# Performance work log

Hardware: AMD Instinct MI355X
Metric: run time of the kernel (lower is better)

The kernel has to match this reference:

```python
import jax, jax.numpy as jnp
import numpy as np

I3 = jnp.eye(3, dtype=jnp.float32)
G_VEC = jnp.array([0.0, 0.0, -9.80665], dtype=jnp.float32)
# Q diag: [cov_omega x3, cov_acc x3, cov_b_omega x3, cov_b_acc x3, cov_Rot_c_i x3, cov_t_c_i x3]
Q_DIAG = jnp.array([1e-3] * 3 + [1e-2] * 3 + [6e-9] * 3 + [2e-4] * 3 + [1e-9] * 3 + [1e-9] * 3, dtype=jnp.float32)
N_NORM_ROT = 100
N_NORM_ROT_CI = 1000


def skew(v):
    z = jnp.zeros_like(v[0])
    return jnp.stack([jnp.stack([z, -v[2], v[1]]),
                      jnp.stack([v[2], z, -v[0]]),
                      jnp.stack([-v[1], v[0], z])])


def so3exp(phi):
    a2 = jnp.sum(phi * phi)
    small = a2 < 1e-12
    a = jnp.sqrt(jnp.where(small, 1.0, a2))
    axis = phi / a
    c, s = jnp.cos(a), jnp.sin(a)
    big = c * I3 + (1.0 - c) * jnp.outer(axis, axis) + s * skew(axis)
    return jnp.where(small, I3 + skew(phi), big)


def sen3exp(xi):
    # SE_2(3) exponential: xi[:3]=rotation, xi[3:9]=(v, p) parts
    phi = xi[:3]
    a2 = jnp.sum(phi * phi)
    small = a2 < 1e-12
    a = jnp.sqrt(jnp.where(small, 1.0, a2))
    axis = phi / a
    c, s = jnp.cos(a), jnp.sin(a)
    sk = skew(axis)
    R = jnp.where(small, I3 + skew(phi),
                  c * I3 + (1.0 - c) * jnp.outer(axis, axis) + s * sk)
    J = jnp.where(small, I3 + 0.5 * skew(phi),
                  (s / a) * I3 + (1.0 - s / a) * jnp.outer(axis, axis) + ((1.0 - c) / a) * sk)
    x = J @ xi[3:].reshape(2, 3).T  # (3,2): columns are dv, dp
    return R, x


def normalize_rot(R):
    # Polar-factor re-orthonormalization (equivalent to the SVD-based
    # normalize_rot for near-rotation matrices), via Newton-Schulz iteration
    # which is smooth and jit/vjp friendly.
    def body(X, _):
        return 1.5 * X - 0.5 * (X @ X.T @ X), None
    X, _ = jax.lax.scan(body, R, None, length=8)
    return X


def from_rpy(roll, pitch, yaw):
    cr, sr = jnp.cos(roll), jnp.sin(roll)
    cp, sp = jnp.cos(pitch), jnp.sin(pitch)
    cy, sy = jnp.cos(yaw), jnp.sin(yaw)
    one = jnp.ones_like(cr)
    zero = jnp.zeros_like(cr)
    Rx = jnp.stack([jnp.stack([one, zero, zero]), jnp.stack([zero, cr, -sr]), jnp.stack([zero, sr, cr])])
    Ry = jnp.stack([jnp.stack([cp, zero, sp]), jnp.stack([zero, one, zero]), jnp.stack([-sp, zero, cp])])
    Rz = jnp.stack([jnp.stack([cy, -sy, zero]), jnp.stack([sy, cy, zero]), jnp.stack([zero, zero, one])])
    return Rz @ Ry @ Rx


def init_covariance():
    P = jnp.zeros((21, 21), dtype=jnp.float32)
    P = P.at[:2, :2].set(1e-3 * jnp.eye(2))     # cov_Rot0 (no yaw error)
    P = P.at[3:5, 3:5].set(0.1 * jnp.eye(2))    # cov_v0
    P = P.at[9:12, 9:12].set(6e-3 * I3)         # cov_b_omega0
    P = P.at[12:15, 12:15].set(4e-3 * I3)       # cov_b_acc0
    P = P.at[15:18, 15:18].set(1e-6 * I3)       # cov_Rot_c_i0
    P = P.at[18:21, 18:21].set(5e-3 * I3)       # cov_t_c_i0
    return P


def propagate_cov(P, Rot, v, p, dt):
    F = jnp.zeros((21, 21), dtype=P.dtype)
    F = F.at[3:6, :3].set(skew(G_VEC))
    F = F.at[6:9, 3:6].set(I3)
    F = F.at[:3, 9:12].set(-Rot)
    F = F.at[3:6, 9:12].set(-skew(v) @ Rot)
    F = F.at[3:6, 12:15].set(-Rot)
    F = F.at[6:9, 9:12].set(-skew(p) @ Rot)
    G = jnp.zeros((21, 18), dtype=P.dtype)
    G = G.at[:3, :3].set(Rot)
    G = G.at[3:6, 3:6].set(Rot)
    G = G.at[9:12, 6:9].set(I3)
    G = G.at[12:15, 9:12].set(I3)
    G = G.at[15:18, 12:15].set(I3)
    G = G.at[18:21, 15:18].set(I3)
    F = F * dt
    G = G * dt
    F2 = F @ F
    Phi = jnp.eye(21, dtype=P.dtype) + F + 0.5 * F2 + (F2 @ F) / 6.0  # 3rd-order expm
    return Phi @ (P + (G * Q_DIAG[None, :]) @ G.T) @ Phi.T


def _step(carry, xs):
    Rot, v, p, b_om, b_ac, Rci, tci, P = carry
    u_i, dt_i, mcov_i, i = xs
    # ---- propagate ----
    acc = Rot @ (u_i[3:6] - b_ac) + G_VEC
    v_n = v + acc * dt_i
    p_n = p + v * dt_i + 0.5 * acc * dt_i * dt_i
    Rot_n = Rot @ so3exp((u_i[:3] - b_om) * dt_i)
    P_n = propagate_cov(P, Rot, v, p, dt_i)
    # ---- update: zero lateral/vertical body-velocity pseudo-measurement ----
    omega = u_i[:3] - b_om
    Rot_body = Rot_n @ Rci
    v_imu = Rot_n.T @ v_n
    v_body = Rci.T @ v_imu + skew(tci) @ omega
    H = jnp.zeros((2, 21), dtype=P.dtype)
    H = H.at[:, 3:6].set(Rot_body.T[1:])
    H = H.at[:, 15:18].set((Rci.T @ skew(v_imu))[1:])
    H = H.at[:, 9:12].set(skew(tci)[1:])
    H = H.at[:, 18:21].set(-skew(omega)[1:])
    r = -v_body[1:]
    Rm = jnp.diag(mcov_i)
    S = H @ P_n @ H.T + Rm                    # (2,2)
    K = jnp.linalg.solve(S, H @ P_n).T        # K = P H^T S^-1 (P, S symmetric)
    dx = K @ r                                 # (21,)
    dR, dxi = sen3exp(dx[:9])
    Rot_u = dR @ Rot_n
    v_u = dR @ v_n + dxi[:, 0]
    p_u = dR @ p_n + dxi[:, 1]
    b_om_u = b_om + dx[9:12]
    b_ac_u = b_ac + dx[12:15]
    Rci_u = so3exp(dx[15:18]) @ Rci
    tci_u = tci + dx[18:21]
    IKH = jnp.eye(21, dtype=P.dtype) - K @ H
    P_u = IKH @ P_n @ IKH.T + K @ Rm @ K.T    # Joseph form
    P_u = 0.5 * (P_u + P_u.T)
    Rot_u = jnp.where(i % N_NORM_ROT == 0, normalize_rot(Rot_u), Rot_u)
    Rci_u = jnp.where(i % N_NORM_ROT_CI == 0, normalize_rot(Rci_u), Rci_u)
    carry = (Rot_u, v_u, p_u, b_om_u, b_ac_u, Rci_u, tci_u, P_u)
    return carry, (Rot_u, v_u, p_u, b_om_u, b_ac_u, Rci_u, tci_u)


def _forward(t, u, measurements_covs, v_mes, p_mes, ang0, N):
    dt = t[1:N] - t[:N - 1]
    Rot0 = from_rpy(ang0[0], ang0[1], ang0[2])
    z3 = jnp.zeros(3, dtype=u.dtype)
    carry0 = (Rot0, v_mes[0], z3, z3, z3, I3, z3, init_covariance())
    xs = (u[1:N], dt, measurements_covs[1:N], jnp.arange(1, N))
    _, ys = jax.lax.scan(_step, carry0, xs)
    Rot = jnp.concatenate([Rot0[None], ys[0]], axis=0)
    v = jnp.concatenate([v_mes[0][None], ys[1]], axis=0)
    p = jnp.concatenate([z3[None], ys[2]], axis=0)
    b_omega = jnp.concatenate([z3[None], ys[3]], axis=0)
    b_acc = jnp.concatenate([z3[None], ys[4]], axis=0)
    Rot_c_i = jnp.concatenate([I3[None], ys[5]], axis=0)
    t_c_i = jnp.concatenate([z3[None], ys[6]], axis=0)
    return (Rot, v, p, b_omega, b_acc, Rot_c_i, t_c_i)


def setup_inputs() -> dict:
    key = jax.random.key(0)
    N = 20000  # 200 s at 100 Hz IMU
    k0, k1, k2, k3, k4, k5 = jax.random.split(key, 6)
    t = jnp.arange(N, dtype=jnp.float32) * 0.01
    gyro = 0.01 * jax.random.normal(k0, (N, 3), dtype=jnp.float32)
    acc = jnp.array([0.0, 0.0, 9.80665], jnp.float32) + 0.1 * jax.random.normal(k1, (N, 3), dtype=jnp.float32)
    u = jnp.concatenate([gyro, acc], axis=1)
    measurements_covs = 0.1 + jax.random.uniform(k2, (N, 2), dtype=jnp.float32)
    v_mes = jax.random.normal(k3, (N, 3), dtype=jnp.float32)
    p_mes = jax.random.normal(k4, (N, 3), dtype=jnp.float32)
    ang0 = 0.01 * jax.random.normal(k5, (3,), dtype=jnp.float32)
    return dict(t=t, u=u, measurements_covs=measurements_covs, v_mes=v_mes, p_mes=p_mes, ang0=ang0, N=N)


def reference(t, u, measurements_covs, v_mes, p_mes, ang0, N):
    return _forward(t, u, measurements_covs, v_mes, p_mes, ang0, N)
```

## Files before the change

kernel.cpp:

```cpp
#include <hip/hip_runtime.h>

#define GRAV 9.80665f
#define WAVE_SYNC() do { \
    asm volatile("s_waitcnt lgkmcnt(0)" ::: "memory"); \
    __builtin_amdgcn_sched_barrier(0); \
  } while(0)

__device__ __forceinline__ float sel3(int r, float a0, float a1, float a2){
  float x = (r==1)? a1 : a0;
  return (r>=2)? a2 : x;
}

__device__ __forceinline__ void mm33(float* __restrict__ O, const float* A, const float* B){
#pragma unroll
  for(int r=0;r<3;++r){
#pragma unroll
    for(int c=0;c<3;++c){
      O[r*3+c] = A[r*3+0]*B[0*3+c] + A[r*3+1]*B[1*3+c] + A[r*3+2]*B[2*3+c];
    }
  }
}

__device__ __forceinline__ void rot_from_t2(float t_, float p0, float p1, float p2, float* R){
  float c_, k1_, k2_;
  if (t_ < 1e-4f){
    c_  = 1.f - t_*(0.5f - t_*((1.f/24.f) - t_*(1.f/720.f)));
    k2_ = 1.f - t_*((1.f/6.f) - t_*((1.f/120.f) - t_*(1.f/5040.f)));
    k1_ = 0.5f - t_*((1.f/24.f) - t_*(1.f/720.f));
  } else {
    float a = sqrtf(t_);
    c_ = __cosf(a);
    float s = __sinf(a);
    k2_ = s/a;
    k1_ = (1.f - c_)/t_;
  }
  R[0]=c_+k1_*p0*p0;      R[1]=k1_*p0*p1-k2_*p2;  R[2]=k1_*p0*p2+k2_*p1;
  R[3]=k1_*p0*p1+k2_*p2;  R[4]=c_+k1_*p1*p1;      R[5]=k1_*p1*p2-k2_*p0;
  R[6]=k1_*p0*p2-k2_*p1;  R[7]=k1_*p1*p2+k2_*p0;  R[8]=c_+k1_*p2*p2;
}

__device__ __forceinline__ void normalize_rot9(float* X){
#pragma unroll 1
  for(int it=0; it<8; ++it){
    float Y[9], Z[9];
#pragma unroll
    for(int r=0;r<3;++r)
#pragma unroll
      for(int c=0;c<3;++c)
        Y[r*3+c] = X[r*3+0]*X[c*3+0] + X[r*3+1]*X[c*3+1] + X[r*3+2]*X[c*3+2];
#pragma unroll
    for(int r=0;r<3;++r)
#pragma unroll
      for(int c=0;c<3;++c)
        Z[r*3+c] = Y[r*3+0]*X[0*3+c] + Y[r*3+1]*X[1*3+c] + Y[r*3+2]*X[2*3+c];
#pragma unroll
    for(int e=0;e<9;++e) X[e] = 1.5f*X[e] - 0.5f*Z[e];
  }
}

__device__ __forceinline__ float pick_state(int l,
    const float* Rt, const float* vv, const float* pp,
    const float* bw, const float* ba, const float* Rc, const float* tc){
  float s = Rt[0];
  s=(l==1)?Rt[1]:s;  s=(l==2)?Rt[2]:s;  s=(l==3)?Rt[3]:s;  s=(l==4)?Rt[4]:s;
  s=(l==5)?Rt[5]:s;  s=(l==6)?Rt[6]:s;  s=(l==7)?Rt[7]:s;  s=(l==8)?Rt[8]:s;
  s=(l==9)?vv[0]:s;  s=(l==10)?vv[1]:s; s=(l==11)?vv[2]:s;
  s=(l==12)?pp[0]:s; s=(l==13)?pp[1]:s; s=(l==14)?pp[2]:s;
  s=(l==15)?bw[0]:s; s=(l==16)?bw[1]:s; s=(l==17)?bw[2]:s;
  s=(l==18)?ba[0]:s; s=(l==19)?ba[1]:s; s=(l==20)?ba[2]:s;
  s=(l==21)?Rc[0]:s; s=(l==22)?Rc[1]:s; s=(l==23)?Rc[2]:s;
  s=(l==24)?Rc[3]:s; s=(l==25)?Rc[4]:s; s=(l==26)?Rc[5]:s;
  s=(l==27)?Rc[6]:s; s=(l==28)?Rc[7]:s; s=(l==29)?Rc[8]:s;
  s=(l==30)?tc[0]:s; s=(l==31)?tc[1]:s; s=(l==32)?tc[2]:s;
  return s;
}

__global__ __launch_bounds__(64,1)
void iekf_scan_kernel(const float* __restrict__ t,
                      const float* __restrict__ u,
                      const float* __restrict__ mcov,
                      const float* __restrict__ v_mes,
                      const float* __restrict__ ang0,
                      float* __restrict__ out, int N)
{
  const int l = threadIdx.x;
  __shared__ float  Pm[441];
  __shared__ float  Eb[441];
  __shared__ float  PnS[441];
  __shared__ float2 HPs2[21];

  float Rt[9], vv[3], pp[3], bw[3], ba[3], Rc[9], tc[3];
  {
    float rl = ang0[0], pt = ang0[1], yw = ang0[2];
    float cr=cosf(rl), sr=sinf(rl), cp=cosf(pt), sp=sinf(pt), cy=cosf(yw), sy=sinf(yw);
    Rt[0]=cy*cp; Rt[1]=cy*sp*sr - sy*cr; Rt[2]=cy*sp*cr + sy*sr;
    Rt[3]=sy*cp; Rt[4]=sy*sp*sr + cy*cr; Rt[5]=sy*sp*cr - cy*sr;
    Rt[6]=-sp;   Rt[7]=cp*sr;            Rt[8]=cp*cr;
  }
  vv[0]=v_mes[0]; vv[1]=v_mes[1]; vv[2]=v_mes[2];
#pragma unroll
  for(int k=0;k<3;++k){ pp[k]=0.f; bw[k]=0.f; ba[k]=0.f; tc[k]=0.f; }
  Rc[0]=1.f;Rc[1]=0.f;Rc[2]=0.f;Rc[3]=0.f;Rc[4]=1.f;Rc[5]=0.f;Rc[6]=0.f;Rc[7]=0.f;Rc[8]=1.f;

  for (int e=l; e<441; e+=64){
    int r=e/21, c=e-(e/21)*21;
    float vI=0.f;
    if (r==c){
      if (r<2) vI=0.001f;
      else if (r==3||r==4) vI=0.1f;
      else if (r>=9&&r<12) vI=0.006f;
      else if (r>=12&&r<15) vI=0.004f;
      else if (r>=15&&r<18) vI=1e-6f;
      else if (r>=18) vI=0.005f;
    }
    Pm[e]=vI;
  }

  int ostr=0; float* op = out;
  {
    int obase=0, ooff=0;
    if (l<9)       {obase=0;    ostr=9; ooff=l;}
    else if (l<12) {obase=9*N;  ostr=3; ooff=l-9;}
    else if (l<15) {obase=12*N; ostr=3; ooff=l-12;}
    else if (l<18) {obase=15*N; ostr=3; ooff=l-15;}
    else if (l<21) {obase=18*N; ostr=3; ooff=l-18;}
    else if (l<30) {obase=21*N; ostr=9; ooff=l-21;}
    else           {obase=30*N; ostr=3; ooff=l-30;}
    op = out + obase + ooff;
  }

  const int g21 = l/21;
  const int c21 = l - g21*21;
  const int cw  = 9 + 4*g21;
  int l1 = l+21; if (l1>=63) l1-=63;
  int l2 = l+42; if (l2>=63) l2-=63;

  static const int cols[12] = {3,4,5, 9,10,11, 15,16,17, 18,19,20};

  {
    float sv = pick_state(l, Rt, vv, pp, bw, ba, Rc, tc);
    if (l<33) op[0] = sv;
  }
  __syncthreads();

  float tA = t[0], tB = t[1];
  float cu[6];
#pragma unroll
  for(int k=0;k<6;++k) cu[k]=u[6+k];
  float cm0=mcov[2], cm1=mcov[3];

  int nx100=100, nx1000=1000;

#pragma unroll 1
  for (int i=1; i<N; ++i){
    float dt = tB - tA;
    float u0=cu[0], u1=cu[1], u2=cu[2], u3=cu[3], u4=cu[4], u5=cu[5];
    float crm0=cm0, crm1=cm1;
    if (i+1 < N){
      tA = tB; tB = t[i+1];
#pragma unroll
      for(int k=0;k<6;++k) cu[k]=u[(i+1)*6+k];
      cm0 = mcov[(i+1)*2]; cm1 = mcov[(i+1)*2+1];
    }
    float dt2=dt*dt, gdt=GRAV*dt, hdt=0.5f*dt, g6=gdt*dt*(1.0f/6.0f), hdt2=0.5f*dt*dt;

    float w0=u0-bw[0], w1=u1-bw[1], w2=u2-bw[2];
    float aa0=u3-ba[0], aa1=u4-ba[1], aa2=u5-ba[2];
    float acc0 = Rt[0]*aa0+Rt[1]*aa1+Rt[2]*aa2;
    float acc1 = Rt[3]*aa0+Rt[4]*aa1+Rt[5]*aa2;
    float acc2 = Rt[6]*aa0+Rt[7]*aa1+Rt[8]*aa2 - GRAV;
    float vn0=vv[0]+acc0*dt, vn1=vv[1]+acc1*dt, vn2=vv[2]+acc2*dt;
    float pn0=pp[0]+vv[0]*dt+acc0*hdt2;
    float pn1=pp[1]+vv[1]*dt+acc1*hdt2;
    float pn2=pp[2]+vv[2]*dt+acc2*hdt2;
    float ph0=w0*dt, ph1=w1*dt, ph2=w2*dt;
    float dRs[9]; rot_from_t2(ph0*ph0+ph1*ph1+ph2*ph2, ph0,ph1,ph2, dRs);
    float Rn[9]; mm33(Rn, Rt, dRs);
    float Rb[9]; mm33(Rb, Rn, Rc);
    float vi0 = Rn[0]*vn0+Rn[3]*vn1+Rn[6]*vn2;
    float vi1 = Rn[1]*vn0+Rn[4]*vn1+Rn[7]*vn2;
    float vi2 = Rn[2]*vn0+Rn[5]*vn1+Rn[8]*vn2;
    float vb1 = Rc[1]*vi0+Rc[4]*vi1+Rc[7]*vi2 + (tc[2]*w0 - tc[0]*w2);
    float vb2 = Rc[2]*vi0+Rc[5]*vi1+Rc[8]*vi2 + (tc[0]*w1 - tc[1]*w0);
    float rr0 = -vb1, rr1 = -vb2;

    float H0[12], H1[12];
    H0[0]=Rb[1]; H0[1]=Rb[4]; H0[2]=Rb[7];
    H1[0]=Rb[2]; H1[1]=Rb[5]; H1[2]=Rb[8];
    H0[3]=tc[2];  H0[4]=0.f;   H0[5]=-tc[0];
    H1[3]=-tc[1]; H1[4]=tc[0]; H1[5]=0.f;
    H0[6]=Rc[4]*vi2 - Rc[7]*vi1;  H0[7]=Rc[7]*vi0 - Rc[1]*vi2;  H0[8]=Rc[1]*vi1 - Rc[4]*vi0;
    H1[6]=Rc[5]*vi2 - Rc[8]*vi1;  H1[7]=Rc[8]*vi0 - Rc[2]*vi2;  H1[8]=Rc[2]*vi1 - Rc[5]*vi0;
    H0[9]=-w2; H0[10]=0.f; H0[11]=w0;
    H1[9]=w1;  H1[10]=-w0; H1[11]=0.f;

    float Bm[9], Cab[9], D2a[9];
#pragma unroll
    for(int k=0;k<3;++k){
      float b0=-dt*Rt[k], b1=-dt*Rt[3+k], b2=-dt*Rt[6+k];
      float c0=dt*(vv[2]*Rt[3+k]-vv[1]*Rt[6+k]);
      float c1=dt*(vv[0]*Rt[6+k]-vv[2]*Rt[k]);
      float c2=dt*(vv[1]*Rt[k]-vv[0]*Rt[3+k]);
      float d0=dt*(pp[2]*Rt[3+k]-pp[1]*Rt[6+k]);
      float d1=dt*(pp[0]*Rt[6+k]-pp[2]*Rt[k]);
      float d2=dt*(pp[1]*Rt[k]-pp[0]*Rt[3+k]);
      Bm[k]=b0; Bm[3+k]=b1; Bm[6+k]=b2;
      Cab[k]=c0+0.5f*gdt*b1; Cab[3+k]=c1-0.5f*gdt*b0; Cab[6+k]=c2;
      D2a[k]=d0+hdt*c0+g6*b1; D2a[3+k]=d1+hdt*c1-g6*b0; D2a[6+k]=d2+hdt*c2;
    }
    float Bs0=sel3(g21,Bm[0],Bm[3],Bm[6]),  Bs1=sel3(g21,Bm[1],Bm[4],Bm[7]),  Bs2=sel3(g21,Bm[2],Bm[5],Bm[8]);
    float Cs0=sel3(g21,Cab[0],Cab[3],Cab[6]),Cs1=sel3(g21,Cab[1],Cab[4],Cab[7]),Cs2=sel3(g21,Cab[2],Cab[5],Cab[8]);
    float Ds0=sel3(g21,D2a[0],D2a[3],D2a[6]),Ds1=sel3(g21,D2a[1],D2a[4],D2a[7]),Ds2=sel3(g21,D2a[2],D2a[5],D2a[8]);

    float RRT00=Rt[0]*Rt[0]+Rt[1]*Rt[1]+Rt[2]*Rt[2];
    float RRT01=Rt[0]*Rt[3]+Rt[1]*Rt[4]+Rt[2]*Rt[5];
    float RRT02=Rt[0]*Rt[6]+Rt[1]*Rt[7]+Rt[2]*Rt[8];
    float RRT11=Rt[3]*Rt[3]+Rt[4]*Rt[4]+Rt[5]*Rt[5];
    float RRT12=Rt[3]*Rt[6]+Rt[4]*Rt[7]+Rt[5]*Rt[8];
    float RRT22=Rt[6]*Rt[6]+Rt[7]*Rt[7]+Rt[8]*Rt[8];
    float q0d=0.001f*dt2, q1d=0.01f*dt2;
    float q69=6e-9f*dt2, q24=2e-4f*dt2, q19=1e-9f*dt2;

    if (l<63){
      int c = c21;
      bool cl3 = (c<3);
      bool c36 = (c>=3 && c<6);
      float R0c  = sel3(c,   RRT00, RRT01, RRT02);
      float R1c  = sel3(c,   RRT01, RRT11, RRT12);
      float R2c  = sel3(c,   RRT02, RRT12, RRT22);
      float R0c3 = sel3(c-3, RRT00, RRT01, RRT02);
      float R1c3 = sel3(c-3, RRT01, RRT11, RRT12);
      float R2c3 = sel3(c-3, RRT02, RRT12, RRT22);
      float d0  = cl3 ? q0d*R0c : 0.f;
      float d1  = cl3 ? q0d*R1c : 0.f;
      float dg  = cl3 ? q0d*sel3(g21,R0c,R1c,R2c) : 0.f;
      float dg3 = c36 ? q1d*sel3(g21,R0c3,R1c3,R2c3) : 0.f;

      float m0  = Pm[c]            + d0;
      float m1  = Pm[21+c]         + d1;
      float mr  = Pm[g21*21+c]     + dg;
      float m3r = Pm[(3+g21)*21+c] + dg3;
      float m6r = Pm[(6+g21)*21+c];
      float m9  = Pm[9*21+c]  + ((c==9) ? q69 : 0.f);
      float m10 = Pm[10*21+c] + ((c==10)? q69 : 0.f);
      float m11 = Pm[11*21+c] + ((c==11)? q69 : 0.f);
      float m12 = Pm[12*21+c] + ((c==12)? q24 : 0.f);
      float m13 = Pm[13*21+c] + ((c==13)? q24 : 0.f);
      float m14 = Pm[14*21+c] + ((c==14)? q24 : 0.f);

      float Ar = (g21==0)? gdt*m1 : (g21==1)? -gdt*m0 : 0.f;
      float bterm = Bs0*m12+Bs1*m13+Bs2*m14;
      float e0 = mr + Bs0*m9+Bs1*m10+Bs2*m11;
      float e1 = m3r + Ar + Cs0*m9+Cs1*m10+Cs2*m11 + bterm;
      float e2 = m6r + hdt*Ar + dt*m3r + Ds0*m9+Ds1*m10+Ds2*m11 + hdt*bterm;
      Eb[g21*21+c]=e0; Eb[(3+g21)*21+c]=e1; Eb[(6+g21)*21+c]=e2;
#pragma unroll
      for (int jj=0;jj<4;++jj){
        int row = cw+jj;
        float qd = (row<12)? q69 : (row<15)? q24 : q19;
        Eb[row*21+c] = Pm[row*21+c] + ((row==c)? qd : 0.f);
      }
    }
    WAVE_SYNC();

    float pnv[7];
#pragma unroll
    for(int k=0;k<7;++k) pnv[k]=0.f;
    float p0=0.f, p1=0.f;
    if (l<63){
      int r = c21;
      const float* Er = Eb + r*21;
      float e0a=Er[0], e1a=Er[1];
      float eg=Er[g21], e3g=Er[3+g21], e6g=Er[6+g21];
      float e9=Er[9],e10=Er[10],e11=Er[11],e12=Er[12],e13=Er[13],e14=Er[14];
      float Ag = (g21==0)? gdt*e1a : (g21==1)? -gdt*e0a : 0.f;
      float bterm = Bs0*e12+Bs1*e13+Bs2*e14;
      pnv[0] = eg + Bs0*e9+Bs1*e10+Bs2*e11;
      pnv[1] = e3g + Ag + Cs0*e9+Cs1*e10+Cs2*e11 + bterm;
      pnv[2] = e6g + hdt*Ag + dt*e3g + Ds0*e9+Ds1*e10+Ds2*e11 + hdt*bterm;
      pnv[3] = Er[cw]; pnv[4] = Er[cw+1]; pnv[5] = Er[cw+2]; pnv[6] = Er[cw+3];

      PnS[r*21 + g21]     = pnv[0];
      PnS[r*21 + 3+g21]   = pnv[1];
      PnS[r*21 + 6+g21]   = pnv[2];
      PnS[r*21 + cw]      = pnv[3];
      PnS[r*21 + cw+1]    = pnv[4];
      PnS[r*21 + cw+2]    = pnv[5];
      PnS[r*21 + cw+3]    = pnv[6];

      float c1a = sel3(g21, H0[0], H0[1], H0[2]);
      float c3a = sel3(g21, H0[3], 0.f,   H0[8]);
      float c4a = sel3(g21, H0[4], 0.f,   H0[9]);
      float c5a = sel3(g21, H0[5], H0[6], H0[10]);
      float c6a = sel3(g21, 0.f,   H0[7], H0[11]);
      float c1b = sel3(g21, H1[0], H1[1], H1[2]);
      float c3b = sel3(g21, H1[3], 0.f,   H1[8]);
      float c4b = sel3(g21, H1[4], 0.f,   H1[9]);
      float c5b = sel3(g21, H1[5], H1[6], H1[10]);
      float c6b = sel3(g21, 0.f,   H1[7], H1[11]);
      p0 = c1a*pnv[1] + c3a*pnv[3] + c4a*pnv[4] + c5a*pnv[5] + c6a*pnv[6];
      p1 = c1b*pnv[1] + c3b*pnv[3] + c4b*pnv[4] + c5b*pnv[5] + c6b*pnv[6];
    }
    float hpr0 = p0 + __shfl(p0, l1) + __shfl(p0, l2);
    float hpr1 = p1 + __shfl(p1, l1) + __shfl(p1, l2);
    if (l<21) HPs2[c21] = make_float2(hpr0, hpr1);
    WAVE_SYNC();

    float hph00=0.f, hph01=0.f, hph10=0.f, hph11=0.f;
#pragma unroll
    for(int k=0;k<12;++k){
      float2 hp = HPs2[cols[k]];
      hph00 += hp.x*H0[k]; hph01 += hp.x*H1[k];
      hph10 += hp.y*H0[k]; hph11 += hp.y*H1[k];
    }
    float s00 = hph00 + crm0, s01 = hph01, s10 = hph10, s11 = hph11 + crm1;
    float idet = 1.0f/(s00*s11 - s01*s10);
    float i00 =  s11*idet, i01 = -s01*idet, i10 = -s10*idet, i11 = s00*idet;
    float K0 = i00*hpr0 + i01*hpr1;
    float K1 = i10*hpr0 + i11*hpr1;
    float s01q = 0.5f*(s01 + s10);
    float dxval = K0*rr0 + K1*rr1;
    float dxr[21];
    {
      int db = __float_as_int(dxval);
#pragma unroll
      for (int k=0;k<21;++k) dxr[k] = __int_as_float(__builtin_amdgcn_readlane(db, k));
    }

    if (l<63){
      int r = c21;
#pragma unroll
      for (int s=0;s<7;++s){
        int j = (s<3)? (g21 + 3*s) : (cw + (s-3));
        float pnT = PnS[j*21 + r];
        float2 hpj = HPs2[j];
        float kjx = i00*hpj.x + i01*hpj.y;
        float kjy = i10*hpj.x + i11*hpj.y;
        float base  = 0.5f*(pnv[s] + pnT);
        float cross = (K0*hpj.x + K1*hpj.y) + (kjx*hpr0 + kjy*hpr1);
        float quad  = (K0*kjx)*s00 + (K0*kjy + K1*kjx)*s01q + (K1*kjy)*s11;
        Pm[r*21+j] = base - cross + quad;
      }
    }

    float t2x = dxr[0]*dxr[0]+dxr[1]*dxr[1]+dxr[2]*dxr[2];
    float cX,k1X,k2X,j1X;
    if (t2x < 1e-4f){
      cX  = 1.f - t2x*(0.5f - t2x*((1.f/24.f) - t2x*(1.f/720.f)));
      k2X = 1.f - t2x*((1.f/6.f) - t2x*((1.f/120.f) - t2x*(1.f/5040.f)));
      k1X = 0.5f - t2x*((1.f/24.f) - t2x*(1.f/720.f));
      j1X = (1.f/6.f) - t2x*((1.f/120.f) - t2x*(1.f/5040.f));
    } else {
      float a = sqrtf(t2x);
      cX = __cosf(a);
      float s = __sinf(a);
      k2X = s/a; k1X = (1.f-cX)/t2x; j1X = (1.f-k2X)/t2x;
    }
    float dR[9];
    dR[0]=cX+k1X*dxr[0]*dxr[0];      dR[1]=k1X*dxr[0]*dxr[1]-k2X*dxr[2]; dR[2]=k1X*dxr[0]*dxr[2]+k2X*dxr[1];
    dR[3]=k1X*dxr[0]*dxr[1]+k2X*dxr[2]; dR[4]=cX+k1X*dxr[1]*dxr[1];      dR[5]=k1X*dxr[1]*dxr[2]-k2X*dxr[0];
    dR[6]=k1X*dxr[0]*dxr[2]-k2X*dxr[1]; dR[7]=k1X*dxr[1]*dxr[2]+k2X*dxr[0]; dR[8]=cX+k1X*dxr[2]*dxr[2];
    float Jm[9];
    Jm[0]=k2X+j1X*dxr[0]*dxr[0];      Jm[1]=j1X*dxr[0]*dxr[1]-k1X*dxr[2]; Jm[2]=j1X*dxr[0]*dxr[2]+k1X*dxr[1];
    Jm[3]=j1X*dxr[0]*dxr[1]+k1X*dxr[2]; Jm[4]=k2X+j1X*dxr[1]*dxr[1];      Jm[5]=j1X*dxr[1]*dxr[2]-k1X*dxr[0];
    Jm[6]=j1X*dxr[0]*dxr[2]-k1X*dxr[1]; Jm[7]=j1X*dxr[1]*dxr[2]+k1X*dxr[0]; Jm[8]=k2X+j1X*dxr[2]*dxr[2];

    float Ru[9]; mm33(Ru, dR, Rn);
    float vu0 = dR[0]*vn0+dR[1]*vn1+dR[2]*vn2 + Jm[0]*dxr[3]+Jm[1]*dxr[4]+Jm[2]*dxr[5];
    float vu1 = dR[3]*vn0+dR[4]*vn1+dR[5]*vn2 + Jm[3]*dxr[3]+Jm[4]*dxr[4]+Jm[5]*dxr[5];
    float vu2 = dR[6]*vn0+dR[7]*vn1+dR[8]*vn2 + Jm[6]*dxr[3]+Jm[7]*dxr[4]+Jm[8]*dxr[5];
    float pu0 = dR[0]*pn0+dR[1]*pn1+dR[2]*pn2 + Jm[0]*dxr[6]+Jm[1]*dxr[7]+Jm[2]*dxr[8];
    float pu1 = dR[3]*pn0+dR[4]*pn1+dR[5]*pn2 + Jm[3]*dxr[6]+Jm[4]*dxr[7]+Jm[5]*dxr[8];
    float pu2 = dR[6]*pn0+dR[7]*pn1+dR[8]*pn2 + Jm[6]*dxr[6]+Jm[7]*dxr[7]+Jm[8]*dxr[8];
    bw[0]+=dxr[9];  bw[1]+=dxr[10]; bw[2]+=dxr[11];
    ba[0]+=dxr[12]; ba[1]+=dxr[13]; ba[2]+=dxr[14];
    float Ec[9]; rot_from_t2(dxr[15]*dxr[15]+dxr[16]*dxr[16]+dxr[17]*dxr[17], dxr[15],dxr[16],dxr[17], Ec);
    float Rcu[9]; mm33(Rcu, Ec, Rc);
    tc[0]+=dxr[18]; tc[1]+=dxr[19]; tc[2]+=dxr[20];

    if (i==nx100){ normalize_rot9(Ru); nx100+=100; }
    if (i==nx1000){ normalize_rot9(Rcu); nx1000+=1000; }

#pragma unroll
    for(int k=0;k<9;++k){ Rt[k]=Ru[k]; Rc[k]=Rcu[k]; }
    vv[0]=vu0; vv[1]=vu1; vv[2]=vu2;
    pp[0]=pu0; pp[1]=pu1; pp[2]=pu2;

    WAVE_SYNC();

    float sv = pick_state(l, Rt, vv, pp, bw, ba, Rc, tc);
    if (l<33) op[i*ostr] = sv;
  }
}

extern "C" void kernel_launch(void* const* d_in, const int* in_sizes, int n_in,
                              void* d_out, int out_size, void* d_ws, size_t ws_size,
                              hipStream_t stream) {
  (void)n_in; (void)out_size; (void)d_ws; (void)ws_size;
  const float* t     = (const float*)d_in[0];
  const float* u     = (const float*)d_in[1];
  const float* mcov  = (const float*)d_in[2];
  const float* v_mes = (const float*)d_in[3];
  const float* ang0  = (const float*)d_in[5];
  int N = in_sizes[0];
  iekf_scan_kernel<<<dim3(1), dim3(64), 0, stream>>>(t, u, mcov, v_mes, ang0, (float*)d_out, N);
}
```

Measured before the change: 45.60 ms.

## Split filter step across two wavefronts: state propagation vs covariance update

Launches 128 threads as two wavefronts. One wavefront propagates the state, builds H and later applies the correction, while the other computes the covariance propagation and the Kalman update. State, H and the innovation terms now pass through shared memory, with two block-wide barriers per step in place of wave-local syncs. The aim is to run the serial state math alongside the covariance work, at the cost of __syncthreads latency and extra LDS traffic on each of the 20k sequential steps.

```diff
diff --git a/kernel.cpp b/kernel.cpp
--- a/kernel.cpp
+++ b/kernel.cpp
@@ -9,6 +9,19 @@
 __device__ __forceinline__ float sel3(int r, float a0, float a1, float a2){
   float x = (r==1)? a1 : a0;
   return (r>=2)? a2 : x;
+}
+__device__ __forceinline__ float pick12(int k, const float* H){
+  float s=H[0];
+  s=(k==1)?H[1]:s; s=(k==2)?H[2]:s; s=(k==3)?H[3]:s; s=(k==4)?H[4]:s;
+  s=(k==5)?H[5]:s; s=(k==6)?H[6]:s; s=(k==7)?H[7]:s; s=(k==8)?H[8]:s;
+  s=(k==9)?H[9]:s; s=(k==10)?H[10]:s; s=(k==11)?H[11]:s;
+  return s;
+}
+__device__ __forceinline__ float pick9(int k, const float* X){
+  float s=X[0];
+  s=(k==1)?X[1]:s; s=(k==2)?X[2]:s; s=(k==3)?X[3]:s; s=(k==4)?X[4]:s;
+  s=(k==5)?X[5]:s; s=(k==6)?X[6]:s; s=(k==7)?X[7]:s; s=(k==8)?X[8]:s;
+  return s;
 }
 
 __device__ __forceinline__ void mm33(float* __restrict__ O, const float* A, const float* B){
@@ -75,7 +88,7 @@
   return s;
 }
 
-__global__ __launch_bounds__(64,1)
+__global__ __launch_bounds__(128,1)
 void iekf_scan_kernel(const float* __restrict__ t,
                       const float* __restrict__ u,
                       const float* __restrict__ mcov,
@@ -83,26 +96,18 @@
                       const float* __restrict__ ang0,
                       float* __restrict__ out, int N)
 {
-  const int l = threadIdx.x;
+  const int tid = threadIdx.x;
+  const bool isA = (tid < 64);
+  const int l = tid & 63;
+
   __shared__ float  Pm[441];
   __shared__ float  Eb[441];
   __shared__ float  PnS[441];
   __shared__ float2 HPs2[21];
-
-  float Rt[9], vv[3], pp[3], bw[3], ba[3], Rc[9], tc[3];
-  {
-    float rl = ang0[0], pt = ang0[1], yw = ang0[2];
-    float cr=cosf(rl), sr=sinf(rl), cp=cosf(pt), sp=sinf(pt), cy=cosf(yw), sy=sinf(yw);
-    Rt[0]=cy*cp; Rt[1]=cy*sp*sr - sy*cr; Rt[2]=cy*sp*cr + sy*sr;
-    Rt[3]=sy*cp; Rt[4]=sy*sp*sr + cy*cr; Rt[5]=sy*sp*cr - cy*sr;
-    Rt[6]=-sp;   Rt[7]=cp*sr;            Rt[8]=cp*cr;
-  }
-  vv[0]=v_mes[0]; vv[1]=v_mes[1]; vv[2]=v_mes[2];
-#pragma unroll
-  for(int k=0;k<3;++k){ pp[k]=0.f; bw[k]=0.f; ba[k]=0.f; tc[k]=0.f; }
-  Rc[0]=1.f;Rc[1]=0.f;Rc[2]=0.f;Rc[3]=0.f;Rc[4]=1.f;Rc[5]=0.f;Rc[6]=0.f;Rc[7]=0.f;Rc[8]=1.f;
-
-  for (int e=l; e<441; e+=64){
+  __shared__ __align__(16) float stS[36];
+  __shared__ __align__(16) float Hds[24];
+
+  for (int e=tid; e<441; e+=128){
     int r=e/21, c=e-(e/21)*21;
     float vI=0.f;
     if (r==c){
@@ -134,262 +139,376 @@
   const int cw  = 9 + 4*g21;
   int l1 = l+21; if (l1>=63) l1-=63;
   int l2 = l+42; if (l2>=63) l2-=63;
-
   static const int cols[12] = {3,4,5, 9,10,11, 15,16,17, 18,19,20};
 
-  {
-    float sv = pick_state(l, Rt, vv, pp, bw, ba, Rc, tc);
-    if (l<33) op[0] = sv;
+  float tA=0.f, tB=0.f, cu[6]={0,0,0,0,0,0}, cm0=0.f, cm1=0.f;
+
+  if (isA){
+    float Rt0[9], vv0[3], pp0[3], bw0a[3], ba0a[3], Rc0[9], tc0a[3];
+    {
+      float rl = ang0[0], pt = ang0[1], yw = ang0[2];
+      float cr=cosf(rl), sr=sinf(rl), cp=cosf(pt), sp=sinf(pt), cy=cosf(yw), sy=sinf(yw);
+      Rt0[0]=cy*cp; Rt0[1]=cy*sp*sr - sy*cr; Rt0[2]=cy*sp*cr + sy*sr;
+      Rt0[3]=sy*cp; Rt0[4]=sy*sp*sr + cy*cr; Rt0[5]=sy*sp*cr - cy*sr;
+      Rt0[6]=-sp;   Rt0[7]=cp*sr;            Rt0[8]=cp*cr;
+    }
+    vv0[0]=v_mes[0]; vv0[1]=v_mes[1]; vv0[2]=v_mes[2];
+#pragma unroll
+    for(int k=0;k<3;++k){ pp0[k]=0.f; bw0a[k]=0.f; ba0a[k]=0.f; tc0a[k]=0.f; }
+    Rc0[0]=1.f;Rc0[1]=0.f;Rc0[2]=0.f;Rc0[3]=0.f;Rc0[4]=1.f;Rc0[5]=0.f;Rc0[6]=0.f;Rc0[7]=0.f;Rc0[8]=1.f;
+
+    float sv = pick_state(l, Rt0, vv0, pp0, bw0a, ba0a, Rc0, tc0a);
+    if (l<33){ op[0] = sv; stS[l] = sv; }
+
+    tA = t[0]; tB = t[1];
+#pragma unroll
+    for(int k=0;k<6;++k) cu[k]=u[6+k];
+    cm0 = mcov[2]; cm1 = mcov[3];
+    if (l>=33 && l<36) stS[l] = sel3(l-33, tB-tA, cm0, cm1);
   }
   __syncthreads();
-
-  float tA = t[0], tB = t[1];
-  float cu[6];
-#pragma unroll
-  for(int k=0;k<6;++k) cu[k]=u[6+k];
-  float cm0=mcov[2], cm1=mcov[3];
 
   int nx100=100, nx1000=1000;
 
 #pragma unroll 1
   for (int i=1; i<N; ++i){
-    float dt = tB - tA;
-    float u0=cu[0], u1=cu[1], u2=cu[2], u3=cu[3], u4=cu[4], u5=cu[5];
-    float crm0=cm0, crm1=cm1;
-    if (i+1 < N){
-      tA = tB; tB = t[i+1];
-#pragma unroll
-      for(int k=0;k<6;++k) cu[k]=u[(i+1)*6+k];
-      cm0 = mcov[(i+1)*2]; cm1 = mcov[(i+1)*2+1];
+    float Rn[9]; float vn0=0,vn1=0,vn2=0, pn0=0,pn1=0,pn2=0;
+    float H0[12], H1[12];
+    float rr0=0, rr1=0, crm0=0, crm1=0;
+    float bw0=0,bw1=0,bw2=0, ba0=0,ba1=0,ba2=0, tc0=0,tc1=0,tc2=0;
+    float Rc[9];
+    float Bs0=0,Bs1=0,Bs2=0,Cs0=0,Cs1=0,Cs2=0,Ds0=0,Ds1=0,Ds2=0;
+    float dt=0, gdt=0, hdt=0;
+    float pnv[7]; float hpr0=0, hpr1=0;
+#pragma unroll
+    for(int k=0;k<7;++k) pnv[k]=0.f;
+#pragma unroll
+    for(int k=0;k<9;++k){ Rn[k]=0.f; Rc[k]=0.f; }
+#pragma unroll
+    for(int k=0;k<12;++k){ H0[k]=0.f; H1[k]=0.f; }
+
+    if (isA){
+      dt = tB - tA;
+      float u0=cu[0], u1=cu[1], u2=cu[2], u3=cu[3], u4=cu[4], u5=cu[5];
+      crm0=cm0; crm1=cm1;
+      if (i+1 < N){
+        tA = tB; tB = t[i+1];
+#pragma unroll
+        for(int k=0;k<6;++k) cu[k]=u[(i+1)*6+k];
+        cm0 = mcov[(i+1)*2]; cm1 = mcov[(i+1)*2+1];
+      }
+      const float4* st4 = (const float4*)stS;
+      float4 q0=st4[0], q1=st4[1], q2=st4[2], q3=st4[3], q4=st4[4], q5=st4[5], q6=st4[6], q7=st4[7], q8=st4[8];
+      float Rt[9] = {q0.x,q0.y,q0.z,q0.w,q1.x,q1.y,q1.z,q1.w,q2.x};
+      float vv0s=q2.y, vv1s=q2.z, vv2s=q2.w;
+      float pp0s=q3.x, pp1s=q3.y, pp2s=q3.z;
+      bw0=q3.w; bw1=q4.x; bw2=q4.y;
+      ba0=q4.z; ba1=q4.w; ba2=q5.x;
+      Rc[0]=q5.y; Rc[1]=q5.z; Rc[2]=q5.w; Rc[3]=q6.x; Rc[4]=q6.y; Rc[5]=q6.z;
+      Rc[6]=q6.w; Rc[7]=q7.x; Rc[8]=q7.y;
+      tc0=q7.z; tc1=q7.w; tc2=q8.x;
+
+      float hdt2 = 0.5f*dt*dt;
+      float w0=u0-bw0, w1=u1-bw1, w2=u2-bw2;
+      float aa0=u3-ba0, aa1=u4-ba1, aa2=u5-ba2;
+      float acc0 = Rt[0]*aa0+Rt[1]*aa1+Rt[2]*aa2;
+      float acc1 = Rt[3]*aa0+Rt[4]*aa1+Rt[5]*aa2;
+      float acc2 = Rt[6]*aa0+Rt[7]*aa1+Rt[8]*aa2 - GRAV;
+      vn0=vv0s+acc0*dt; vn1=vv1s+acc1*dt; vn2=vv2s+acc2*dt;
+      pn0=pp0s+vv0s*dt+acc0*hdt2;
+      pn1=pp1s+vv1s*dt+acc1*hdt2;
+      pn2=pp2s+vv2s*dt+acc2*hdt2;
+      float ph0=w0*dt, ph1=w1*dt, ph2=w2*dt;
+      float dRs[9]; rot_from_t2(ph0*ph0+ph1*ph1+ph2*ph2, ph0,ph1,ph2, dRs);
+      mm33(Rn, Rt, dRs);
+      float Rb[9]; mm33(Rb, Rn, Rc);
+      float vi0 = Rn[0]*vn0+Rn[3]*vn1+Rn[6]*vn2;
+      float vi1 = Rn[1]*vn0+Rn[4]*vn1+Rn[7]*vn2;
+      float vi2 = Rn[2]*vn0+Rn[5]*vn1+Rn[8]*vn2;
+      float vb1 = Rc[1]*vi0+Rc[4]*vi1+Rc[7]*vi2 + (tc2*w0 - tc0*w2);
+      float vb2 = Rc[2]*vi0+Rc[5]*vi1+Rc[8]*vi2 + (tc0*w1 - tc1*w0);
+      rr0 = -vb1; rr1 = -vb2;
+
+      H0[0]=Rb[1]; H0[1]=Rb[4]; H0[2]=Rb[7];
+      H1[0]=Rb[2]; H1[1]=Rb[5]; H1[2]=Rb[8];
+      H0[3]=tc2;  H0[4]=0.f;  H0[5]=-tc0;
+      H1[3]=-tc1; H1[4]=tc0;  H1[5]=0.f;
+      H0[6]=Rc[4]*vi2 - Rc[7]*vi1;  H0[7]=Rc[7]*vi0 - Rc[1]*vi2;  H0[8]=Rc[1]*vi1 - Rc[4]*vi0;
+      H1[6]=Rc[5]*vi2 - Rc[8]*vi1;  H1[7]=Rc[8]*vi0 - Rc[2]*vi2;  H1[8]=Rc[2]*vi1 - Rc[5]*vi0;
+      H0[9]=-w2; H0[10]=0.f; H0[11]=w0;
+      H1[9]=w1;  H1[10]=-w0; H1[11]=0.f;
+
+      if (l<24){
+        float hv = (l<12)? pick12(l,H0) : pick12(l-12,H1);
+        Hds[l] = hv;
+      }
+    } else {
+      const float4* st4 = (const float4*)stS;
+      float4 q0=st4[0], q1=st4[1], q2=st4[2], q3=st4[3], q8=st4[8];
+      float Rt[9] = {q0.x,q0.y,q0.z,q0.w,q1.x,q1.y,q1.z,q1.w,q2.x};
+      float vv0s=q2.y, vv1s=q2.z, vv2s=q2.w;
+      float pp0s=q3.x, pp1s=q3.y, pp2s=q3.z;
+      dt = q8.y; crm0 = q8.z; crm1 = q8.w;
+      float dt2=dt*dt; gdt=GRAV*dt; hdt=0.5f*dt;
+      float g6=gdt*dt*(1.0f/6.0f);
+
+      float Bm[9], Cab[9], D2a[9];
+#pragma unroll
+      for(int k=0;k<3;++k){
+        float b0=-dt*Rt[k], b1=-dt*Rt[3+k], b2=-dt*Rt[6+k];
+        float c0=dt*(vv2s*Rt[3+k]-vv1s*Rt[6+k]);
+        float c1=dt*(vv0s*Rt[6+k]-vv2s*Rt[k]);
+        float c2=dt*(vv1s*Rt[k]-vv0s*Rt[3+k]);
+        float d0=dt*(pp2s*Rt[3+k]-pp1s*Rt[6+k]);
+        float d1=dt*(pp0s*Rt[6+k]-pp2s*Rt[k]);
+        float d2=dt*(pp1s*Rt[k]-pp0s*Rt[3+k]);
+        Bm[k]=b0; Bm[3+k]=b1; Bm[6+k]=b2;
+        Cab[k]=c0+0.5f*gdt*b1; Cab[3+k]=c1-0.5f*gdt*b0; Cab[6+k]=c2;
+        D2a[k]=d0+hdt*c0+g6*b1; D2a[3+k]=d1+hdt*c1-g6*b0; D2a[6+k]=d2+hdt*c2;
+      }
+      Bs0=sel3(g21,Bm[0],Bm[3],Bm[6]);  Bs1=sel3(g21,Bm[1],Bm[4],Bm[7]);  Bs2=sel3(g21,Bm[2],Bm[5],Bm[8]);
+      Cs0=sel3(g21,Cab[0],Cab[3],Cab[6]);Cs1=sel3(g21,Cab[1],Cab[4],Cab[7]);Cs2=sel3(g21,Cab[2],Cab[5],Cab[8]);
+      Ds0=sel3(g21,D2a[0],D2a[3],D2a[6]);Ds1=sel3(g21,D2a[1],D2a[4],D2a[7]);Ds2=sel3(g21,D2a[2],D2a[5],D2a[8]);
+
+      float RRT00=Rt[0]*Rt[0]+Rt[1]*Rt[1]+Rt[2]*Rt[2];
+      float RRT01=Rt[0]*Rt[3]+Rt[1]*Rt[4]+Rt[2]*Rt[5];
+      float RRT02=Rt[0]*Rt[6]+Rt[1]*Rt[7]+Rt[2]*Rt[8];
+      float RRT11=Rt[3]*Rt[3]+Rt[4]*Rt[4]+Rt[5]*Rt[5];
+      float RRT12=Rt[3]*Rt[6]+Rt[4]*Rt[7]+Rt[5]*Rt[8];
+      float RRT22=Rt[6]*Rt[6]+Rt[7]*Rt[7]+Rt[8]*Rt[8];
+      float q0d=0.001f*dt2, q1d=0.01f*dt2;
+      float q69=6e-9f*dt2, q24=2e-4f*dt2, q19=1e-9f*dt2;
+
+      if (l<63){
+        int c = c21;
+        bool cl3 = (c<3);
+        bool c36 = (c>=3 && c<6);
+        float R0c  = sel3(c,   RRT00, RRT01, RRT02);
+        float R1c  = sel3(c,   RRT01, RRT11, RRT12);
+        float R2c  = sel3(c,   RRT02, RRT12, RRT22);
+        float R0c3 = sel3(c-3, RRT00, RRT01, RRT02);
+        float R1c3 = sel3(c-3, RRT01, RRT11, RRT12);
+        float R2c3 = sel3(c-3, RRT02, RRT12, RRT22);
+        float d0  = cl3 ? q0d*R0c : 0.f;
+        float d1  = cl3 ? q0d*R1c : 0.f;
+        float dg  = cl3 ? q0d*sel3(g21,R0c,R1c,R2c) : 0.f;
+        float dg3 = c36 ? q1d*sel3(g21,R0c3,R1c3,R2c3) : 0.f;
+
+        float m0  = Pm[c]            + d0;
+        float m1  = Pm[21+c]         + d1;
+        float mr  = Pm[g21*21+c]     + dg;
+        float m3r = Pm[(3+g21)*21+c] + dg3;
+        float m6r = Pm[(6+g21)*21+c];
+        float m9  = Pm[9*21+c]  + ((c==9) ? q69 : 0.f);
+        float m10 = Pm[10*21+c] + ((c==10)? q69 : 0.f);
+        float m11 = Pm[11*21+c] + ((c==11)? q69 : 0.f);
+        float m12 = Pm[12*21+c] + ((c==12)? q24 : 0.f);
+        float m13 = Pm[13*21+c] + ((c==13)? q24 : 0.f);
+        float m14 = Pm[14*21+c] + ((c==14)? q24 : 0.f);
+
+        float Ar = (g21==0)? gdt*m1 : (g21==1)? -gdt*m0 : 0.f;
+        float bterm = Bs0*m12+Bs1*m13+Bs2*m14;
+        float e0 = mr + Bs0*m9+Bs1*m10+Bs2*m11;
+        float e1 = m3r + Ar + Cs0*m9+Cs1*m10+Cs2*m11 + bterm;
+        float e2 = m6r + hdt*Ar + dt*m3r + Ds0*m9+Ds1*m10+Ds2*m11 + hdt*bterm;
+        Eb[g21*21+c]=e0; Eb[(3+g21)*21+c]=e1; Eb[(6+g21)*21+c]=e2;
+#pragma unroll
+        for (int jj=0;jj<4;++jj){
+          int row = cw+jj;
+          float qd = (row<12)? q69 : (row<15)? q24 : q19;
+          Eb[row*21+c] = Pm[row*21+c] + ((row==c)? qd : 0.f);
+        }
+      }
     }
-    float dt2=dt*dt, gdt=GRAV*dt, hdt=0.5f*dt, g6=gdt*dt*(1.0f/6.0f), hdt2=0.5f*dt*dt;
-
-    float w0=u0-bw[0], w1=u1-bw[1], w2=u2-bw[2];
-    float aa0=u3-ba[0], aa1=u4-ba[1], aa2=u5-ba[2];
-    float acc0 = Rt[0]*aa0+Rt[1]*aa1+Rt[2]*aa2;
-    float acc1 = Rt[3]*aa0+Rt[4]*aa1+Rt[5]*aa2;
-    float acc2 = Rt[6]*aa0+Rt[7]*aa1+Rt[8]*aa2 - GRAV;
-    float vn0=vv[0]+acc0*dt, vn1=vv[1]+acc1*dt, vn2=vv[2]+acc2*dt;
-    float pn0=pp[0]+vv[0]*dt+acc0*hdt2;
-    float pn1=pp[1]+vv[1]*dt+acc1*hdt2;
-    float pn2=pp[2]+vv[2]*dt+acc2*hdt2;
-    float ph0=w0*dt, ph1=w1*dt, ph2=w2*dt;
-    float dRs[9]; rot_from_t2(ph0*ph0+ph1*ph1+ph2*ph2, ph0,ph1,ph2, dRs);
-    float Rn[9]; mm33(Rn, Rt, dRs);
-    float Rb[9]; mm33(Rb, Rn, Rc);
-    float vi0 = Rn[0]*vn0+Rn[3]*vn1+Rn[6]*vn2;
-    float vi1 = Rn[1]*vn0+Rn[4]*vn1+Rn[7]*vn2;
-    float vi2 = Rn[2]*vn0+Rn[5]*vn1+Rn[8]*vn2;
-    float vb1 = Rc[1]*vi0+Rc[4]*vi1+Rc[7]*vi2 + (tc[2]*w0 - tc[0]*w2);
-    float vb2 = Rc[2]*vi0+Rc[5]*vi1+Rc[8]*vi2 + (tc[0]*w1 - tc[1]*w0);
-    float rr0 = -vb1, rr1 = -vb2;
-
-    float H0[12], H1[12];
-    H0[0]=Rb[1]; H0[1]=Rb[4]; H0[2]=Rb[7];
-    H1[0]=Rb[2]; H1[1]=Rb[5]; H1[2]=Rb[8];
-    H0[3]=tc[2];  H0[4]=0.f;   H0[5]=-tc[0];
-    H1[3]=-tc[1]; H1[4]=tc[0]; H1[5]=0.f;
-    H0[6]=Rc[4]*vi2 - Rc[7]*vi1;  H0[7]=Rc[7]*vi0 - Rc[1]*vi2;  H0[8]=Rc[1]*vi1 - Rc[4]*vi0;
-    H1[6]=Rc[5]*vi2 - Rc[8]*vi1;  H1[7]=Rc[8]*vi0 - Rc[2]*vi2;  H1[8]=Rc[2]*vi1 - Rc[5]*vi0;
-    H0[9]=-w2; H0[10]=0.f; H0[11]=w0;
-    H1[9]=w1;  H1[10]=-w0; H1[11]=0.f;
-
-    float Bm[9], Cab[9], D2a[9];
-#pragma unroll
-    for(int k=0;k<3;++k){
-      float b0=-dt*Rt[k], b1=-dt*Rt[3+k], b2=-dt*Rt[6+k];
-      float c0=dt*(vv[2]*Rt[3+k]-vv[1]*Rt[6+k]);
-      float c1=dt*(vv[0]*Rt[6+k]-vv[2]*Rt[k]);
-      float c2=dt*(vv[1]*Rt[k]-vv[0]*Rt[3+k]);
-      float d0=dt*(pp[2]*Rt[3+k]-pp[1]*Rt[6+k]);
-      float d1=dt*(pp[0]*Rt[6+k]-pp[2]*Rt[k]);
-      float d2=dt*(pp[1]*Rt[k]-pp[0]*Rt[3+k]);
-      Bm[k]=b0; Bm[3+k]=b1; Bm[6+k]=b2;
-      Cab[k]=c0+0.5f*gdt*b1; Cab[3+k]=c1-0.5f*gdt*b0; Cab[6+k]=c2;
-      D2a[k]=d0+hdt*c0+g6*b1; D2a[3+k]=d1+hdt*c1-g6*b0; D2a[6+k]=d2+hdt*c2;
+    __syncthreads();
+
+    if (!isA){
+      const float4* h4p = (const float4*)Hds;
+      float4 h0v=h4p[0], h1v=h4p[1], h2v=h4p[2], h3v=h4p[3], h4v=h4p[4], h5v=h4p[5];
+      H0[0]=h0v.x; H0[1]=h0v.y; H0[2]=h0v.z; H0[3]=h0v.w;
+      H0[4]=h1v.x; H0[5]=h1v.y; H0[6]=h1v.z; H0[7]=h1v.w;
+      H0[8]=h2v.x; H0[9]=h2v.y; H0[10]=h2v.z; H0[11]=h2v.w;
+      H1[0]=h3v.x; H1[1]=h3v.y; H1[2]=h3v.z; H1[3]=h3v.w;
+      H1[4]=h4v.x; H1[5]=h4v.y; H1[6]=h4v.z; H1[7]=h4v.w;
+      H1[8]=h5v.x; H1[9]=h5v.y; H1[10]=h5v.z; H1[11]=h5v.w;
+
+      float p0=0.f, p1=0.f;
+      if (l<63){
+        int r = c21;
+        const float* Er = Eb + r*21;
+        float e0a=Er[0], e1a=Er[1];
+        float eg=Er[g21], e3g=Er[3+g21], e6g=Er[6+g21];
+        float e9=Er[9],e10=Er[10],e11=Er[11],e12=Er[12],e13=Er[13],e14=Er[14];
+        float Ag = (g21==0)? gdt*e1a : (g21==1)? -gdt*e0a : 0.f;
+        float bterm = Bs0*e12+Bs1*e13+Bs2*e14;
+        pnv[0] = eg + Bs0*e9+Bs1*e10+Bs2*e11;
+        pnv[1] = e3g + Ag + Cs0*e9+Cs1*e10+Cs2*e11 + bterm;
+        pnv[2] = e6g + hdt*Ag + dt*e3g + Ds0*e9+Ds1*e10+Ds2*e11 + hdt*bterm;
+        pnv[3] = Er[cw]; pnv[4] = Er[cw+1]; pnv[5] = Er[cw+2]; pnv[6] = Er[cw+3];
+
+        PnS[r*21 + g21]   = pnv[0];
+        PnS[r*21 + 3+g21] = pnv[1];
+        PnS[r*21 + 6+g21] = pnv[2];
+        PnS[r*21 + cw]    = pnv[3];
+        PnS[r*21 + cw+1]  = pnv[4];
+        PnS[r*21 + cw+2]  = pnv[5];
+        PnS[r*21 + cw+3]  = pnv[6];
+
+        float c1a = sel3(g21, H0[0], H0[1], H0[2]);
+        float c3a = sel3(g21, H0[3], 0.f,   H0[8]);
+        float c4a = sel3(g21, H0[4], 0.f,   H0[9]);
+        float c5a = sel3(g21, H0[5], H0[6], H0[10]);
+        float c6a = sel3(g21, 0.f,   H0[7], H0[11]);
+        float c1b = sel3(g21, H1[0], H1[1], H1[2]);
+        float c3b = sel3(g21, H1[3], 0.f,   H1[8]);
+        float c4b = sel3(g21, H1[4], 0.f,   H1[9]);
+        float c5b = sel3(g21, H1[5], H1[6], H1[10]);
+        float c6b = sel3(g21, 0.f,   H1[7], H1[11]);
+        p0 = c1a*pnv[1] + c3a*pnv[3] + c4a*pnv[4] + c5a*pnv[5] + c6a*pnv[6];
+        p1 = c1b*pnv[1] + c3b*pnv[3] + c4b*pnv[4] + c5b*pnv[5] + c6b*pnv[6];
+      }
+      hpr0 = p0 + __shfl(p0, l1) + __shfl(p0, l2);
+      hpr1 = p1 + __shfl(p1, l1) + __shfl(p1, l2);
+      if (l<21) HPs2[l] = make_float2(hpr0, hpr1);
     }
-    float Bs0=sel3(g21,Bm[0],Bm[3],Bm[6]),  Bs1=sel3(g21,Bm[1],Bm[4],Bm[7]),  Bs2=sel3(g21,Bm[2],Bm[5],Bm[8]);
-    float Cs0=sel3(g21,Cab[0],Cab[3],Cab[6]),Cs1=sel3(g21,Cab[1],Cab[4],Cab[7]),Cs2=sel3(g21,Cab[2],Cab[5],Cab[8]);
-    float Ds0=sel3(g21,D2a[0],D2a[3],D2a[6]),Ds1=sel3(g21,D2a[1],D2a[4],D2a[7]),Ds2=sel3(g21,D2a[2],D2a[5],D2a[8]);
-
-    float RRT00=Rt[0]*Rt[0]+Rt[1]*Rt[1]+Rt[2]*Rt[2];
-    float RRT01=Rt[0]*Rt[3]+Rt[1]*Rt[4]+Rt[2]*Rt[5];
-    float RRT02=Rt[0]*Rt[6]+Rt[1]*Rt[7]+Rt[2]*Rt[8];
-    float RRT11=Rt[3]*Rt[3]+Rt[4]*Rt[4]+Rt[5]*Rt[5];
-    float RRT12=Rt[3]*Rt[6]+Rt[4]*Rt[7]+Rt[5]*Rt[8];
-    float RRT22=Rt[6]*Rt[6]+Rt[7]*Rt[7]+Rt[8]*Rt[8];
-    float q0d=0.001f*dt2, q1d=0.01f*dt2;
-    float q69=6e-9f*dt2, q24=2e-4f*dt2, q19=1e-9f*dt2;
-
-    if (l<63){
-      int c = c21;
-      bool cl3 = (c<3);
-      bool c36 = (c>=3 && c<6);
-      float R0c  = sel3(c,   RRT00, RRT01, RRT02);
-      float R1c  = sel3(c,   RRT01, RRT11, RRT12);
-      float R2c  = sel3(c,   RRT02, RRT12, RRT22);
-      float R0c3 = sel3(c-3, RRT00, RRT01, RRT02);
-      float R1c3 = sel3(c-3, RRT01, RRT11, RRT12);
-      float R2c3 = sel3(c-3, RRT02, RRT12, RRT22);
-      float d0  = cl3 ? q0d*R0c : 0.f;
-      float d1  = cl3 ? q0d*R1c : 0.f;
-      float dg  = cl3 ? q0d*sel3(g21,R0c,R1c,R2c) : 0.f;
-      float dg3 = c36 ? q1d*sel3(g21,R0c3,R1c3,R2c3) : 0.f;
-
-      float m0  = Pm[c]            + d0;
-      float m1  = Pm[21+c]         + d1;
-      float mr  = Pm[g21*21+c]     + dg;
-      float m3r = Pm[(3+g21)*21+c] + dg3;
-      float m6r = Pm[(6+g21)*21+c];
-      float m9  = Pm[9*21+c]  + ((c==9) ? q69 : 0.f);
-      float m10 = Pm[10*21+c] + ((c==10)? q69 : 0.f);
-      float m11 = Pm[11*21+c] + ((c==11)? q69 : 0.f);
-      float m12 = Pm[12*21+c] + ((c==12)? q24 : 0.f);
-      float m13 = Pm[13*21+c] + ((c==13)? q24 : 0.f);
-      float m14 = Pm[14*21+c] + ((c==14)? q24 : 0.f);
-
-      float Ar = (g21==0)? gdt*m1 : (g21==1)? -gdt*m0 : 0.f;
-      float bterm = Bs0*m12+Bs1*m13+Bs2*m14;
-      float e0 = mr + Bs0*m9+Bs1*m10+Bs2*m11;
-      float e1 = m3r + Ar + Cs0*m9+Cs1*m10+Cs2*m11 + bterm;
-      float e2 = m6r + hdt*Ar + dt*m3r + Ds0*m9+Ds1*m10+Ds2*m11 + hdt*bterm;
-      Eb[g21*21+c]=e0; Eb[(3+g21)*21+c]=e1; Eb[(6+g21)*21+c]=e2;
-#pragma unroll
-      for (int jj=0;jj<4;++jj){
-        int row = cw+jj;
-        float qd = (row<12)? q69 : (row<15)? q24 : q19;
-        Eb[row*21+c] = Pm[row*21+c] + ((row==c)? qd : 0.f);
+    __syncthreads();
+
+    if (isA){
+      float2 myhp = HPs2[(l<21)? l : 0];
+      float hph00=0.f, hph01=0.f, hph10=0.f, hph11=0.f;
+#pragma unroll
+      for(int k=0;k<12;++k){
+        float2 hp = HPs2[cols[k]];
+        hph00 += hp.x*H0[k]; hph01 += hp.x*H1[k];
+        hph10 += hp.y*H0[k]; hph11 += hp.y*H1[k];
+      }
+      float s00 = hph00 + crm0, s01 = hph01, s10 = hph10, s11 = hph11 + crm1;
+      float idet = 1.0f/(s00*s11 - s01*s10);
+      float i00 =  s11*idet, i01 = -s01*idet, i10 = -s10*idet, i11 = s00*idet;
+      float K0 = i00*myhp.x + i01*myhp.y;
+      float K1 = i10*myhp.x + i11*myhp.y;
+      float dxval = K0*rr0 + K1*rr1;
+
+      int db = __float_as_int(dxval);
+      float dx0 = __int_as_float(__builtin_amdgcn_readlane(db, 0));
+      float dx1 = __int_as_float(__builtin_amdgcn_readlane(db, 1));
+      float dx2 = __int_as_float(__builtin_amdgcn_readlane(db, 2));
+      float dx3 = __int_as_float(__builtin_amdgcn_readlane(db, 3));
+      float dx4 = __int_as_float(__builtin_amdgcn_readlane(db, 4));
+      float dx5 = __int_as_float(__builtin_amdgcn_readlane(db, 5));
+      float dx6 = __int_as_float(__builtin_amdgcn_readlane(db, 6));
+      float dx7 = __int_as_float(__builtin_amdgcn_readlane(db, 7));
+      float dx8 = __int_as_float(__builtin_amdgcn_readlane(db, 8));
+      float dx15 = __int_as_float(__builtin_amdgcn_readlane(db, 15));
+      float dx16 = __int_as_float(__builtin_amdgcn_readlane(db, 16));
+      float dx17 = __int_as_float(__builtin_amdgcn_readlane(db, 17));
+      int src = (l>=30 && l<33)? (l-12) : ((l>=15 && l<21)? (l-6) : 0);
+      float dxadd = __shfl(dxval, src);
+
+      float t2x = dx0*dx0+dx1*dx1+dx2*dx2;
+      float cX,k1X,k2X,j1X;
+      if (t2x < 1e-4f){
+        cX  = 1.f - t2x*(0.5f - t2x*((1.f/24.f) - t2x*(1.f/720.f)));
+        k2X = 1.f - t2x*((1.f/6.f) - t2x*((1.f/120.f) - t2x*(1.f/5040.f)));
+        k1X = 0.5f - t2x*((1.f/24.f) - t2x*(1.f/720.f));
+        j1X = (1.f/6.f) - t2x*((1.f/120.f) - t2x*(1.f/5040.f));
+      } else {
+        float a = sqrtf(t2x);
+        cX = __cosf(a);
+        float s = __sinf(a);
+        k2X = s/a; k1X = (1.f-cX)/t2x; j1X = (1.f-k2X)/t2x;
+      }
+      float dR[9];
+      dR[0]=cX+k1X*dx0*dx0;      dR[1]=k1X*dx0*dx1-k2X*dx2; dR[2]=k1X*dx0*dx2+k2X*dx1;
+      dR[3]=k1X*dx0*dx1+k2X*dx2; dR[4]=cX+k1X*dx1*dx1;      dR[5]=k1X*dx1*dx2-k2X*dx0;
+      dR[6]=k1X*dx0*dx2-k2X*dx1; dR[7]=k1X*dx1*dx2+k2X*dx0; dR[8]=cX+k1X*dx2*dx2;
+      float Jm[9];
+      Jm[0]=k2X+j1X*dx0*dx0;      Jm[1]=j1X*dx0*dx1-k1X*dx2; Jm[2]=j1X*dx0*dx2+k1X*dx1;
+      Jm[3]=j1X*dx0*dx1+k1X*dx2;  Jm[4]=k2X+j1X*dx1*dx1;     Jm[5]=j1X*dx1*dx2-k1X*dx0;
+      Jm[6]=j1X*dx0*dx2-k1X*dx1;  Jm[7]=j1X*dx1*dx2+k1X*dx0; Jm[8]=k2X+j1X*dx2*dx2;
+      float Ec[9];
+      rot_from_t2(dx15*dx15+dx16*dx16+dx17*dx17, dx15,dx16,dx17, Ec);
+
+      float myval = 0.f;
+      if (l<9){
+        int ro=(l>=6)?2:((l>=3)?1:0); int co=l-3*ro;
+        float d0=sel3(ro,dR[0],dR[3],dR[6]), d1=sel3(ro,dR[1],dR[4],dR[7]), d2=sel3(ro,dR[2],dR[5],dR[8]);
+        float n0=sel3(co,Rn[0],Rn[1],Rn[2]), n1=sel3(co,Rn[3],Rn[4],Rn[5]), n2=sel3(co,Rn[6],Rn[7],Rn[8]);
+        myval = d0*n0 + d1*n1 + d2*n2;
+      } else if (l<15){
+        int j=l-9; bool isv=(j<3); int ro = isv? j : (j-3);
+        float x0 = isv? vn0:pn0, x1 = isv? vn1:pn1, x2 = isv? vn2:pn2;
+        float y0 = isv? dx3:dx6, y1 = isv? dx4:dx7, y2 = isv? dx5:dx8;
+        float d0=sel3(ro,dR[0],dR[3],dR[6]), d1=sel3(ro,dR[1],dR[4],dR[7]), d2=sel3(ro,dR[2],dR[5],dR[8]);
+        float j0=sel3(ro,Jm[0],Jm[3],Jm[6]), j1m=sel3(ro,Jm[1],Jm[4],Jm[7]), j2m=sel3(ro,Jm[2],Jm[5],Jm[8]);
+        myval = d0*x0 + d1*x1 + d2*x2 + j0*y0 + j1m*y1 + j2m*y2;
+      } else if (l<21){
+        float old = (l<18)? sel3(l-15,bw0,bw1,bw2) : sel3(l-18,ba0,ba1,ba2);
+        myval = old + dxadd;
+      } else if (l<30){
+        int j=l-21; int ro=(j>=6)?2:((j>=3)?1:0); int co=j-3*ro;
+        float e0=sel3(ro,Ec[0],Ec[3],Ec[6]), e1=sel3(ro,Ec[1],Ec[4],Ec[7]), e2=sel3(ro,Ec[2],Ec[5],Ec[8]);
+        float r0=sel3(co,Rc[0],Rc[1],Rc[2]), r1=sel3(co,Rc[3],Rc[4],Rc[5]), r2=sel3(co,Rc[6],Rc[7],Rc[8]);
+        myval = e0*r0 + e1*r1 + e2*r2;
+      } else if (l<33){
+        myval = sel3(l-30,tc0,tc1,tc2) + dxadd;
+      }
+      if (l<33) stS[l] = myval;
+      if (l>=33 && l<36) stS[l] = sel3(l-33, tB-tA, cm0, cm1);
+
+      bool n100 = (i==nx100), n1000 = (i==nx1000);
+      if (n100) nx100 += 100;
+      if (n1000) nx1000 += 1000;
+      if (n100 || n1000){
+        WAVE_SYNC();
+        if (n100){
+          float X[9];
+#pragma unroll
+          for (int k=0;k<9;++k) X[k]=stS[k];
+          normalize_rot9(X);
+          if (l<9){ myval = pick9(l,X); stS[l] = myval; }
+        }
+        if (n1000){
+          float Y[9];
+#pragma unroll
+          for (int k=0;k<9;++k) Y[k]=stS[21+k];
+          normalize_rot9(Y);
+          if (l>=21 && l<30){ myval = pick9(l-21,Y); stS[l] = myval; }
+        }
+      }
+      if (l<33) op[i*ostr] = myval;
+    } else {
+      float hph00=0.f, hph01=0.f, hph10=0.f, hph11=0.f;
+#pragma unroll
+      for(int k=0;k<12;++k){
+        float2 hp = HPs2[cols[k]];
+        hph00 += hp.x*H0[k]; hph01 += hp.x*H1[k];
+        hph10 += hp.y*H0[k]; hph11 += hp.y*H1[k];
+      }
+      float s00 = hph00 + crm0, s01 = hph01, s10 = hph10, s11 = hph11 + crm1;
+      float idet = 1.0f/(s00*s11 - s01*s10);
+      float i00 =  s11*idet, i01 = -s01*idet, i10 = -s10*idet, i11 = s00*idet;
+      float s01q = 0.5f*(s01 + s10);
+      float K0 = i00*hpr0 + i01*hpr1;
+      float K1 = i10*hpr0 + i11*hpr1;
+
+      if (l<63){
+        int r = c21;
+#pragma unroll
+        for (int s=0;s<7;++s){
+          int j = (s<3)? (g21 + 3*s) : (cw + (s-3));
+          float pnT = PnS[j*21 + r];
+          float2 hpj = HPs2[j];
+          float kjx = i00*hpj.x + i01*hpj.y;
+          float kjy = i10*hpj.x + i11*hpj.y;
+          float base  = 0.5f*(pnv[s] + pnT);
+          float cross = (K0*hpj.x + K1*hpj.y) + (kjx*hpr0 + kjy*hpr1);
+          float quad  = (K0*kjx)*s00 + (K0*kjy + K1*kjx)*s01q + (K1*kjy)*s11;
+          Pm[r*21+j] = base - cross + quad;
+        }
       }
     }
-    WAVE_SYNC();
-
-    float pnv[7];
-#pragma unroll
-    for(int k=0;k<7;++k) pnv[k]=0.f;
-    float p0=0.f, p1=0.f;
-    if (l<63){
-      int r = c21;
-      const float* Er = Eb + r*21;
-      float e0a=Er[0], e1a=Er[1];
-      float eg=Er[g21], e3g=Er[3+g21], e6g=Er[6+g21];
-      float e9=Er[9],e10=Er[10],e11=Er[11],e12=Er[12],e13=Er[13],e14=Er[14];
-      float Ag = (g21==0)? gdt*e1a : (g21==1)? -gdt*e0a : 0.f;
-      float bterm = Bs0*e12+Bs1*e13+Bs2*e14;
-      pnv[0] = eg + Bs0*e9+Bs1*e10+Bs2*e11;
-      pnv[1] = e3g + Ag + Cs0*e9+Cs1*e10+Cs2*e11 + bterm;
-      pnv[2] = e6g + hdt*Ag + dt*e3g + Ds0*e9+Ds1*e10+Ds2*e11 + hdt*bterm;
-      pnv[3] = Er[cw]; pnv[4] = Er[cw+1]; pnv[5] = Er[cw+2]; pnv[6] = Er[cw+3];
-
-      PnS[r*21 + g21]     = pnv[0];
-      PnS[r*21 + 3+g21]   = pnv[1];
-      PnS[r*21 + 6+g21]   = pnv[2];
-      PnS[r*21 + cw]      = pnv[3];
-      PnS[r*21 + cw+1]    = pnv[4];
-      PnS[r*21 + cw+2]    = pnv[5];
-      PnS[r*21 + cw+3]    = pnv[6];
-
-      float c1a = sel3(g21, H0[0], H0[1], H0[2]);
-      float c3a = sel3(g21, H0[3], 0.f,   H0[8]);
-      float c4a = sel3(g21, H0[4], 0.f,   H0[9]);
-      float c5a = sel3(g21, H0[5], H0[6], H0[10]);
-      float c6a = sel3(g21, 0.f,   H0[7], H0[11]);
-      float c1b = sel3(g21, H1[0], H1[1], H1[2]);
-      float c3b = sel3(g21, H1[3], 0.f,   H1[8]);
-      float c4b = sel3(g21, H1[4], 0.f,   H1[9]);
-      float c5b = sel3(g21, H1[5], H1[6], H1[10]);
-      float c6b = sel3(g21, 0.f,   H1[7], H1[11]);
-      p0 = c1a*pnv[1] + c3a*pnv[3] + c4a*pnv[4] + c5a*pnv[5] + c6a*pnv[6];
-      p1 = c1b*pnv[1] + c3b*pnv[3] + c4b*pnv[4] + c5b*pnv[5] + c6b*pnv[6];
-    }
-    float hpr0 = p0 + __shfl(p0, l1) + __shfl(p0, l2);
-    float hpr1 = p1 + __shfl(p1, l1) + __shfl(p1, l2);
-    if (l<21) HPs2[c21] = make_float2(hpr0, hpr1);
-    WAVE_SYNC();
-
-    float hph00=0.f, hph01=0.f, hph10=0.f, hph11=0.f;
-#pragma unroll
-    for(int k=0;k<12;++k){
-      float2 hp = HPs2[cols[k]];
-      hph00 += hp.x*H0[k]; hph01 += hp.x*H1[k];
-      hph10 += hp.y*H0[k]; hph11 += hp.y*H1[k];
-    }
-    float s00 = hph00 + crm0, s01 = hph01, s10 = hph10, s11 = hph11 + crm1;
-    float idet = 1.0f/(s00*s11 - s01*s10);
-    float i00 =  s11*idet, i01 = -s01*idet, i10 = -s10*idet, i11 = s00*idet;
-    float K0 = i00*hpr0 + i01*hpr1;
-    float K1 = i10*hpr0 + i11*hpr1;
-    float s01q = 0.5f*(s01 + s10);
-    float dxval = K0*rr0 + K1*rr1;
-    float dxr[21];
-    {
-      int db = __float_as_int(dxval);
-#pragma unroll
-      for (int k=0;k<21;++k) dxr[k] = __int_as_float(__builtin_amdgcn_readlane(db, k));
-    }
-
-    if (l<63){
-      int r = c21;
-#pragma unroll
-      for (int s=0;s<7;++s){
-        int j = (s<3)? (g21 + 3*s) : (cw + (s-3));
-        float pnT = PnS[j*21 + r];
-        float2 hpj = HPs2[j];
-        float kjx = i00*hpj.x + i01*hpj.y;
-        float kjy = i10*hpj.x + i11*hpj.y;
-        float base  = 0.5f*(pnv[s] + pnT);
-        float cross = (K0*hpj.x + K1*hpj.y) + (kjx*hpr0 + kjy*hpr1);
-        float quad  = (K0*kjx)*s00 + (K0*kjy + K1*kjx)*s01q + (K1*kjy)*s11;
-        Pm[r*21+j] = base - cross + quad;
-      }
-    }
-
-    float t2x = dxr[0]*dxr[0]+dxr[1]*dxr[1]+dxr[2]*dxr[2];
-    float cX,k1X,k2X,j1X;
-    if (t2x < 1e-4f){
-      cX  = 1.f - t2x*(0.5f - t2x*((1.f/24.f) - t2x*(1.f/720.f)));
-      k2X = 1.f - t2x*((1.f/6.f) - t2x*((1.f/120.f) - t2x*(1.f/5040.f)));
-      k1X = 0.5f - t2x*((1.f/24.f) - t2x*(1.f/720.f));
-      j1X = (1.f/6.f) - t2x*((1.f/120.f) - t2x*(1.f/5040.f));
-    } else {
-      float a = sqrtf(t2x);
-      cX = __cosf(a);
-      float s = __sinf(a);
-      k2X = s/a; k1X = (1.f-cX)/t2x; j1X = (1.f-k2X)/t2x;
-    }
-    float dR[9];
-    dR[0]=cX+k1X*dxr[0]*dxr[0];      dR[1]=k1X*dxr[0]*dxr[1]-k2X*dxr[2]; dR[2]=k1X*dxr[0]*dxr[2]+k2X*dxr[1];
-    dR[3]=k1X*dxr[0]*dxr[1]+k2X*dxr[2]; dR[4]=cX+k1X*dxr[1]*dxr[1];      dR[5]=k1X*dxr[1]*dxr[2]-k2X*dxr[0];
-    dR[6]=k1X*dxr[0]*dxr[2]-k2X*dxr[1]; dR[7]=k1X*dxr[1]*dxr[2]+k2X*dxr[0]; dR[8]=cX+k1X*dxr[2]*dxr[2];
-    float Jm[9];
-    Jm[0]=k2X+j1X*dxr[0]*dxr[0];      Jm[1]=j1X*dxr[0]*dxr[1]-k1X*dxr[2]; Jm[2]=j1X*dxr[0]*dxr[2]+k1X*dxr[1];
-    Jm[3]=j1X*dxr[0]*dxr[1]+k1X*dxr[2]; Jm[4]=k2X+j1X*dxr[1]*dxr[1];      Jm[5]=j1X*dxr[1]*dxr[2]-k1X*dxr[0];
-    Jm[6]=j1X*dxr[0]*dxr[2]-k1X*dxr[1]; Jm[7]=j1X*dxr[1]*dxr[2]+k1X*dxr[0]; Jm[8]=k2X+j1X*dxr[2]*dxr[2];
-
-    float Ru[9]; mm33(Ru, dR, Rn);
-    float vu0 = dR[0]*vn0+dR[1]*vn1+dR[2]*vn2 + Jm[0]*dxr[3]+Jm[1]*dxr[4]+Jm[2]*dxr[5];
-    float vu1 = dR[3]*vn0+dR[4]*vn1+dR[5]*vn2 + Jm[3]*dxr[3]+Jm[4]*dxr[4]+Jm[5]*dxr[5];
-    float vu2 = dR[6]*vn0+dR[7]*vn1+dR[8]*vn2 + Jm[6]*dxr[3]+Jm[7]*dxr[4]+Jm[8]*dxr[5];
-    float pu0 = dR[0]*pn0+dR[1]*pn1+dR[2]*pn2 + Jm[0]*dxr[6]+Jm[1]*dxr[7]+Jm[2]*dxr[8];
-    float pu1 = dR[3]*pn0+dR[4]*pn1+dR[5]*pn2 + Jm[3]*dxr[6]+Jm[4]*dxr[7]+Jm[5]*dxr[8];
-    float pu2 = dR[6]*pn0+dR[7]*pn1+dR[8]*pn2 + Jm[6]*dxr[6]+Jm[7]*dxr[7]+Jm[8]*dxr[8];
-    bw[0]+=dxr[9];  bw[1]+=dxr[10]; bw[2]+=dxr[11];
-    ba[0]+=dxr[12]; ba[1]+=dxr[13]; ba[2]+=dxr[14];
-    float Ec[9]; rot_from_t2(dxr[15]*dxr[15]+dxr[16]*dxr[16]+dxr[17]*dxr[17], dxr[15],dxr[16],dxr[17], Ec);
-    float Rcu[9]; mm33(Rcu, Ec, Rc);
-    tc[0]+=dxr[18]; tc[1]+=dxr[19]; tc[2]+=dxr[20];
-
-    if (i==nx100){ normalize_rot9(Ru); nx100+=100; }
-    if (i==nx1000){ normalize_rot9(Rcu); nx1000+=1000; }
-
-#pragma unroll
-    for(int k=0;k<9;++k){ Rt[k]=Ru[k]; Rc[k]=Rcu[k]; }
-    vv[0]=vu0; vv[1]=vu1; vv[2]=vu2;
-    pp[0]=pu0; pp[1]=pu1; pp[2]=pu2;
-
-    WAVE_SYNC();
-
-    float sv = pick_state(l, Rt, vv, pp, bw, ba, Rc, tc);
-    if (l<33) op[i*ostr] = sv;
+    __syncthreads();
   }
 }
 
@@ -403,5 +522,5 @@
   const float* v_mes = (const float*)d_in[3];
   const float* ang0  = (const float*)d_in[5];
   int N = in_sizes[0];
-  iekf_scan_kernel<<<dim3(1), dim3(64), 0, stream>>>(t, u, mcov, v_mes, ang0, (float*)d_out, N);
-}
+  iekf_scan_kernel<<<dim3(1), dim3(128), 0, stream>>>(t, u, mcov, v_mes, ang0, (float*)d_out, N);
+}
```

After: 51.56 ms. 13.1% more time.
